# Performance work log

Measured on AMD Instinct MI355X. Metric: run time of the kernel, lower is better.

Reference implementation:

```python
import jax, jax.numpy as jnp
import numpy as np

B, C, G, P, W, H = 16, 64, 256, 4096, 1024, 256
WQ = W // 4  # wsi_dim // 4 = 256
D = C + G + WQ  # concat dim fed to score MLP = 576


def _init_linear(key, fan_in, fan_out):
    k1, k2 = jax.random.split(key)
    bound = 1.0 / np.sqrt(fan_in)
    w = jax.random.uniform(k1, (fan_in, fan_out), jnp.float32, -bound, bound)
    b = jax.random.uniform(k2, (fan_out,), jnp.float32, -bound, bound)
    return w, b


def setup_inputs() -> dict:
    key = jax.random.key(0)
    ks = jax.random.split(key, 8)
    cx = jax.random.normal(ks[0], (B, C), jnp.float32)
    gx = jax.random.normal(ks[1], (B, G), jnp.float32)
    wx = jax.random.normal(ks[2], (B, P, W), jnp.float32)
    Wc, bc = _init_linear(ks[3], C, C)        # fc_c
    Wg, bg = _init_linear(ks[4], G, G)        # fc_g
    Ww, bw = _init_linear(ks[5], W, WQ)       # fc_w
    W1, b1 = _init_linear(ks[6], D, H)        # FCLayers hidden
    W2, b2 = _init_linear(ks[7], H, 1)        # FCLayers out
    return {"cx": cx, "gx": gx, "wx": wx,
            "Wc": Wc, "bc": bc, "Wg": Wg, "bg": bg, "Ww": Ww, "bw": bw,
            "W1": W1, "b1": b1, "W2": W2, "b2": b2}


def reference(cx, gx, wx, Wc, bc, Wg, bg, Ww, bw, W1, b1, W2, b2):
    # Per-modality projections
    c = cx @ Wc + bc                      # [B, C]
    g = gx @ Wg + bg                      # [B, G]
    w = jnp.einsum('bpw,wq->bpq', wx, Ww) + bw  # [B, P, WQ]
    # Score MLP on concat(c, g, w_i) for every patch, vectorized by
    # splitting W1 rows over the concat blocks (avoids materializing concat):
    W1c, W1g, W1w = W1[:C], W1[C:C + G], W1[C + G:]
    h = jax.nn.relu((c @ W1c + g @ W1g + b1)[:, None, :]
                    + jnp.einsum('bpq,qh->bph', w, W1w))  # [B, P, H]
    scores = h @ W2 + b2                  # [B, P, 1]
    attn = jax.nn.softmax(scores, axis=1)  # softmax over patches
    return jnp.sum(attn * w, axis=1)      # [B, WQ]
```

## Files before the change

kernel.cpp:

```cpp
#include <hip/hip_runtime.h>
#include <hip/hip_bf16.h>

#define B_   16
#define C_   64
#define G_   256
#define P_   4096
#define W_   1024
#define H_   256
#define WQ_  256
#define M_   (B_ * P_)

typedef __attribute__((ext_vector_type(8))) _Float16 f16x8;
typedef __attribute__((ext_vector_type(4))) float    f32x4;

__device__ __forceinline__ float h2f(ushort u) {
    union { ushort u; _Float16 h; } cv; cv.u = u;
    return (float)cv.h;
}

#define GLOAD16(gsrc, ldst)                                                  \
    __builtin_amdgcn_global_load_lds(                                        \
        (const __attribute__((address_space(1))) unsigned int*)(gsrc),       \
        (__attribute__((address_space(3))) unsigned int*)(ldst), 16, 0, 0)

__device__ __forceinline__ void convT_dev(
    const float* __restrict__ src, ushort* __restrict__ dst,
    int K, int N, int blk, float* tile )
{
    const int nb = N >> 6;
    const int k0 = (blk / nb) * 64;
    const int n0 = (blk % nb) * 64;
    const int t = threadIdx.x;
    #pragma unroll
    for (int i = 0; i < 16; ++i) {
        int e = i * 256 + t;
        int kr = e >> 6, nc = e & 63;
        tile[nc * 65 + kr] = src[(size_t)(k0 + kr) * N + n0 + nc];
    }
    __syncthreads();
    #pragma unroll
    for (int i = 0; i < 16; ++i) {
        int e = i * 256 + t;
        int nc = e >> 6, kr = e & 63;
        union { _Float16 h; ushort u; } cv;
        cv.h = (_Float16)tile[nc * 65 + kr];
        dst[(size_t)(n0 + nc) * K + k0 + kr] = cv.u;
    }
}

__global__ __launch_bounds__(256) void setup_kernel(
    const float* __restrict__ Ww,  ushort* __restrict__ WwT,
    const float* __restrict__ W1w, ushort* __restrict__ W1T,
    const float* __restrict__ cx, const float* __restrict__ gx,
    const float* __restrict__ Wc, const float* __restrict__ bc,
    const float* __restrict__ Wg, const float* __restrict__ bg,
    const float* __restrict__ W1, const float* __restrict__ b1,
    float* __restrict__ base_out)
{
    __shared__ float smem[64 * 65];
    const int blk = blockIdx.x;
    if (blk < 64) {
        convT_dev(Ww, WwT, W_, WQ_, blk, smem);
        return;
    }
    if (blk < 80) {
        convT_dev(W1w, W1T, H_, H_, blk - 64, smem);
        return;
    }
    const int b = blk - 80;
    const int t = threadIdx.x;
    float* cxl = smem;
    float* gxl = smem + 64;
    float* cl  = smem + 320;
    float* gl  = smem + 384;

    if (t < C_) cxl[t] = cx[b * C_ + t];
    gxl[t] = gx[b * G_ + t];
    __syncthreads();

    if (t < C_) {
        float acc = bc[t];
        #pragma unroll 4
        for (int i = 0; i < C_; ++i) acc += cxl[i] * Wc[i * C_ + t];
        cl[t] = acc;
    }
    {
        float acc = bg[t];
        #pragma unroll 4
        for (int i = 0; i < G_; ++i) acc += gxl[i] * Wg[i * G_ + t];
        gl[t] = acc;
    }
    __syncthreads();

    float acc = b1[t];
    #pragma unroll 4
    for (int i = 0; i < C_; ++i) acc += cl[i] * W1[i * H_ + t];
    #pragma unroll 4
    for (int i = 0; i < G_; ++i) acc += gl[i] * W1[(C_ + i) * H_ + t];
    base_out[b * H_ + t] = acc;
}

__global__ __launch_bounds__(512, 2) void gemm_w_fused(
    const float* __restrict__ A,
    const ushort* __restrict__ BT,
    const float* __restrict__ bw,
    const ushort* __restrict__ W1T,
    const float* __restrict__ base_,
    const float* __restrict__ W2,
    const float* __restrict__ b2,
    ushort* Cout,
    float* __restrict__ scores)
{
    __shared__ __align__(16) char smem[65536];
    float*  Af = (float*)smem;
    ushort* Bh = (ushort*)(smem + 32768);
    ushort* wt = (ushort*)smem;

    const int t = threadIdx.x;
    const int row0 = blockIdx.x * 128;
    const int b = blockIdx.x >> 5;
    const int lane = t & 63, wave = t >> 6;
    const int wm = wave >> 2, wn = wave & 3;
    const int l15 = lane & 15, lq = lane >> 4;

    const float *srcA0, *srcA1, *srcA2, *srcA3;
    char *dstA0, *dstA1, *dstA2, *dstA3;
    {
        const int o0 = t * 16, o1 = o0 + 8192, o2 = o0 + 16384, o3 = o0 + 24576;
        const int r0 = o0 >> 8, r1 = o1 >> 8, r2 = o2 >> 8, r3 = o3 >> 8;
        srcA0 = A + (size_t)(row0 + r0) * W_ + (((o0 & 255) ^ ((r0 & 7) << 4)) >> 2);
        srcA1 = A + (size_t)(row0 + r1) * W_ + (((o1 & 255) ^ ((r1 & 7) << 4)) >> 2);
        srcA2 = A + (size_t)(row0 + r2) * W_ + (((o2 & 255) ^ ((r2 & 7) << 4)) >> 2);
        srcA3 = A + (size_t)(row0 + r3) * W_ + (((o3 & 255) ^ ((r3 & 7) << 4)) >> 2);
        dstA0 = (char*)Af + o0; dstA1 = (char*)Af + o1;
        dstA2 = (char*)Af + o2; dstA3 = (char*)Af + o3;
    }
    const ushort *srcB0, *srcB1, *srcB2, *srcB3;
    char *dstB0, *dstB1, *dstB2, *dstB3;
    {
        const int o0 = t * 16, o1 = o0 + 8192, o2 = o0 + 16384, o3 = o0 + 24576;
        const int c0 = o0 >> 7, c1 = o1 >> 7, c2 = o2 >> 7, c3 = o3 >> 7;
        srcB0 = BT + (size_t)c0 * W_ + (((o0 & 127) ^ ((c0 & 7) << 4)) >> 1);
        srcB1 = BT + (size_t)c1 * W_ + (((o1 & 127) ^ ((c1 & 7) << 4)) >> 1);
        srcB2 = BT + (size_t)c2 * W_ + (((o2 & 127) ^ ((c2 & 7) << 4)) >> 1);
        srcB3 = BT + (size_t)c3 * W_ + (((o3 & 127) ^ ((c3 & 7) << 4)) >> 1);
        dstB0 = (char*)Bh + o0; dstB1 = (char*)Bh + o1;
        dstB2 = (char*)Bh + o2; dstB3 = (char*)Bh + o3;
    }

    f32x4 acc[4][4];
    #pragma unroll
    for (int m = 0; m < 4; ++m)
        #pragma unroll
        for (int n = 0; n < 4; ++n) acc[m][n] = (f32x4){0.f, 0.f, 0.f, 0.f};

    for (int k0 = 0; k0 < W_; k0 += 64) {
        if (k0) __syncthreads();
        GLOAD16(srcA0 + k0, dstA0);
        GLOAD16(srcA1 + k0, dstA1);
        GLOAD16(srcA2 + k0, dstA2);
        GLOAD16(srcA3 + k0, dstA3);
        GLOAD16(srcB0 + k0, dstB0);
        GLOAD16(srcB1 + k0, dstB1);
        GLOAD16(srcB2 + k0, dstB2);
        GLOAD16(srcB3 + k0, dstB3);
        __syncthreads();

        #pragma unroll
        for (int ks = 0; ks < 2; ++ks) {
            f16x8 af[4], bf[4];
            #pragma unroll
            for (int m = 0; m < 4; ++m) {
                const int r = wm * 64 + m * 16 + l15;
                const int base = r * 256 + ks * 128 + lq * 32;
                const int swz  = (r & 7) << 4;
                const f32x4 a0 = *(const f32x4*)((const char*)Af + (base ^ swz));
                const f32x4 a1 = *(const f32x4*)((const char*)Af + ((base + 16) ^ swz));
                f16x8 h;
                h[0] = (_Float16)a0[0]; h[1] = (_Float16)a0[1];
                h[2] = (_Float16)a0[2]; h[3] = (_Float16)a0[3];
                h[4] = (_Float16)a1[0]; h[5] = (_Float16)a1[1];
                h[6] = (_Float16)a1[2]; h[7] = (_Float16)a1[3];
                af[m] = h;
            }
            #pragma unroll
            for (int n = 0; n < 4; ++n) {
                const int c = wn * 64 + n * 16 + l15;
                const int byte = (c * 128 + ks * 64 + lq * 16) ^ ((c & 7) << 4);
                bf[n] = *(const f16x8*)((const char*)Bh + byte);
            }
            #pragma unroll
            for (int m = 0; m < 4; ++m)
                #pragma unroll
                for (int n = 0; n < 4; ++n)
                    acc[m][n] = __builtin_amdgcn_mfma_f32_16x16x32_f16(
                        af[m], bf[n], acc[m][n], 0, 0, 0);
        }
    }

    __syncthreads();
    {
        float bwv[4];
        #pragma unroll
        for (int n = 0; n < 4; ++n) bwv[n] = bw[wn * 64 + n * 16 + l15];
        #pragma unroll
        for (int m = 0; m < 4; ++m)
            #pragma unroll
            for (int reg = 0; reg < 4; ++reg) {
                const int rl = wm * 64 + m * 16 + lq * 4 + reg;
                #pragma unroll
                for (int n = 0; n < 4; ++n) {
                    const int col = wn * 64 + n * 16 + l15;
                    union { _Float16 h; ushort u; } cv;
                    cv.h = (_Float16)(acc[m][n][reg] + bwv[n]);
                    Cout[(size_t)(row0 + rl) * WQ_ + col] = cv.u;
                    *(ushort*)((char*)wt + ((rl * 512 + col * 2) ^ ((rl & 7) << 4))) = cv.u;
                }
            }
    }
    __syncthreads();

    f32x4 acc2[4][4];
    #pragma unroll
    for (int m = 0; m < 4; ++m)
        #pragma unroll
        for (int n = 0; n < 4; ++n) acc2[m][n] = (f32x4){0.f, 0.f, 0.f, 0.f};

    for (int k2 = 0; k2 < WQ_; k2 += 32) {
        f16x8 af[4], bf[4];
        #pragma unroll
        for (int m = 0; m < 4; ++m) {
            const int r = wm * 64 + m * 16 + l15;
            const int byte = (r * 512 + (k2 + lq * 8) * 2) ^ ((r & 7) << 4);
            af[m] = *(const f16x8*)((const char*)wt + byte);
        }
        #pragma unroll
        for (int n = 0; n < 4; ++n) {
            const int c = wn * 64 + n * 16 + l15;
            bf[n] = *(const f16x8*)(W1T + (size_t)c * WQ_ + k2 + lq * 8);
        }
        #pragma unroll
        for (int m = 0; m < 4; ++m)
            #pragma unroll
            for (int n = 0; n < 4; ++n)
                acc2[m][n] = __builtin_amdgcn_mfma_f32_16x16x32_f16(
                    af[m], bf[n], acc2[m][n], 0, 0, 0);
    }

    __syncthreads();
    {
        float (*red2)[128] = (float(*)[128])smem;
        float basev[4], w2v[4];
        #pragma unroll
        for (int n = 0; n < 4; ++n) {
            const int col = wn * 64 + n * 16 + l15;
            basev[n] = base_[b * H_ + col];
            w2v[n] = W2[col];
        }
        #pragma unroll
        for (int m = 0; m < 4; ++m)
            #pragma unroll
            for (int reg = 0; reg < 4; ++reg) {
                float s = 0.f;
                #pragma unroll
                for (int n = 0; n < 4; ++n) {
                    float h = acc2[m][n][reg] + basev[n];
                    h = fmaxf(h, 0.f);
                    s += h * w2v[n];
                }
                s += __shfl_xor(s, 1, 64);
                s += __shfl_xor(s, 2, 64);
                s += __shfl_xor(s, 4, 64);
                s += __shfl_xor(s, 8, 64);
                if (l15 == 0) red2[wn][wm * 64 + m * 16 + lq * 4 + reg] = s;
            }
        __syncthreads();
        if (t < 128) {
            scores[row0 + t] =
                red2[0][t] + red2[1][t] + red2[2][t] + red2[3][t] + b2[0];
        }
    }
}

__global__ __launch_bounds__(256) void weighted_partial_kernel(
    const ushort* __restrict__ wmat16, const float* __restrict__ scores,
    float* __restrict__ part)
{
    const int blk = blockIdx.x;
    const int b   = blk >> 5;
    const int sl  = blk & 31;
    const int t   = threadIdx.x;
    const int rg  = t >> 5;
    const int q8  = (t & 31) * 8;
    __shared__ float red[8][WQ_];
    __shared__ float mred[4];

    float mv = -1e30f;
    for (int p = t; p < P_; p += 256) mv = fmaxf(mv, scores[b * P_ + p]);
    #pragma unroll
    for (int d = 1; d < 64; d <<= 1) mv = fmaxf(mv, __shfl_xor(mv, d, 64));
    if ((t & 63) == 0) mred[t >> 6] = mv;
    __syncthreads();
    const float m = fmaxf(fmaxf(mred[0], mred[1]), fmaxf(mred[2], mred[3]));

    float acc[8];
    #pragma unroll
    for (int j = 0; j < 8; ++j) acc[j] = 0.f;

    const int p0 = sl * 128 + rg * 16;
    for (int p = p0; p < p0 + 16; ++p) {
        const float e = expf(scores[b * P_ + p] - m);
        const uint4 raw = *(const uint4*)(wmat16 + ((size_t)b * P_ + p) * WQ_ + q8);
        const ushort* u = (const ushort*)&raw;
        #pragma unroll
        for (int j = 0; j < 8; ++j) acc[j] += e * h2f(u[j]);
    }
    #pragma unroll
    for (int j = 0; j < 8; ++j) red[rg][q8 + j] = acc[j];
    __syncthreads();
    float s = 0.f;
    #pragma unroll
    for (int g = 0; g < 8; ++g) s += red[g][t];
    part[(size_t)(b * 32 + sl) * WQ_ + t] = s;
}

__global__ __launch_bounds__(256) void finalize_kernel(
    const float* __restrict__ part, const float* __restrict__ scores,
    float* __restrict__ out)
{
    const int b = blockIdx.x;
    const int t = threadIdx.x;
    __shared__ float mred[4];
    __shared__ float zred[4];

    float mv = -1e30f;
    for (int p = t; p < P_; p += 256) mv = fmaxf(mv, scores[b * P_ + p]);
    #pragma unroll
    for (int d = 1; d < 64; d <<= 1) mv = fmaxf(mv, __shfl_xor(mv, d, 64));
    if ((t & 63) == 0) mred[t >> 6] = mv;
    __syncthreads();
    const float m = fmaxf(fmaxf(mred[0], mred[1]), fmaxf(mred[2], mred[3]));

    float zv = 0.f;
    for (int p = t; p < P_; p += 256) zv += expf(scores[b * P_ + p] - m);
    #pragma unroll
    for (int d = 1; d < 64; d <<= 1) zv += __shfl_xor(zv, d, 64);
    if ((t & 63) == 0) zred[t >> 6] = zv;
    __syncthreads();
    const float z = zred[0] + zred[1] + zred[2] + zred[3];

    float acc = 0.f;
    #pragma unroll
    for (int sl = 0; sl < 32; ++sl) acc += part[(size_t)(b * 32 + sl) * WQ_ + t];
    out[b * WQ_ + t] = acc / z;
}

extern "C" void kernel_launch(void* const* d_in, const int* in_sizes, int n_in,
                              void* d_out, int out_size, void* d_ws, size_t ws_size,
                              hipStream_t stream) {
    const float* cx = (const float*)d_in[0];
    const float* gx = (const float*)d_in[1];
    const float* wx = (const float*)d_in[2];
    const float* Wc = (const float*)d_in[3];
    const float* bc = (const float*)d_in[4];
    const float* Wg = (const float*)d_in[5];
    const float* bg = (const float*)d_in[6];
    const float* Ww = (const float*)d_in[7];
    const float* bw = (const float*)d_in[8];
    const float* W1 = (const float*)d_in[9];
    const float* b1 = (const float*)d_in[10];
    const float* W2 = (const float*)d_in[11];
    const float* b2 = (const float*)d_in[12];
    float* out = (float*)d_out;

    float* ws        = (float*)d_ws;
    ushort* ws_w16   = (ushort*)ws;
    float* ws_scores = ws + (size_t)M_ * WQ_ / 2;
    float* ws_base   = ws_scores + M_;
    float* ws_part   = ws_base + B_ * H_;
    ushort* WwT16    = (ushort*)(ws_part + B_ * 32 * WQ_);
    ushort* W1T16    = WwT16 + (size_t)W_ * WQ_;

    setup_kernel<<<96, 256, 0, stream>>>(
        Ww, WwT16, W1 + (size_t)(C_ + G_) * H_, W1T16,
        cx, gx, Wc, bc, Wg, bg, W1, b1, ws_base);

    gemm_w_fused<<<M_ / 128, 512, 0, stream>>>(
        wx, WwT16, bw, W1T16, ws_base, W2, b2, ws_w16, ws_scores);

    weighted_partial_kernel<<<B_ * 32, 256, 0, stream>>>(ws_w16, ws_scores, ws_part);

    finalize_kernel<<<B_, 256, 0, stream>>>(ws_part, ws_scores, out);
}
```

Measured before the change: 177.2 us.

## Double-buffer A/B tiles in fused GEMM with half-depth K stages

```diff
diff --git a/kernel.cpp b/kernel.cpp
--- a/kernel.cpp
+++ b/kernel.cpp
@@ -22,6 +22,13 @@
     __builtin_amdgcn_global_load_lds(                                        \
         (const __attribute__((address_space(1))) unsigned int*)(gsrc),       \
         (__attribute__((address_space(3))) unsigned int*)(ldst), 16, 0, 0)
+
+__device__ __forceinline__ int inv_swz64(int o) {
+    const int b8 = (o >> 8) & 1, b7 = (o >> 7) & 1, b6 = (o >> 6) & 1;
+    const int b5 = (o >> 5) & 1, b4 = (o >> 4) & 1;
+    const int l6 = b6 ^ b8, l5 = b5 ^ b7, l4 = b4 ^ l6;
+    return (o & ~0x70) | (l6 << 6) | (l5 << 5) | (l4 << 4);
+}
 
 __device__ __forceinline__ void convT_dev(
     const float* __restrict__ src, ushort* __restrict__ dst,
@@ -112,8 +119,6 @@
     float* __restrict__ scores)
 {
     __shared__ __align__(16) char smem[65536];
-    float*  Af = (float*)smem;
-    ushort* Bh = (ushort*)(smem + 32768);
     ushort* wt = (ushort*)smem;
 
     const int t = threadIdx.x;
@@ -123,29 +128,25 @@
     const int wm = wave >> 2, wn = wave & 3;
     const int l15 = lane & 15, lq = lane >> 4;
 
-    const float *srcA0, *srcA1, *srcA2, *srcA3;
-    char *dstA0, *dstA1, *dstA2, *dstA3;
-    {
-        const int o0 = t * 16, o1 = o0 + 8192, o2 = o0 + 16384, o3 = o0 + 24576;
-        const int r0 = o0 >> 8, r1 = o1 >> 8, r2 = o2 >> 8, r3 = o3 >> 8;
-        srcA0 = A + (size_t)(row0 + r0) * W_ + (((o0 & 255) ^ ((r0 & 7) << 4)) >> 2);
-        srcA1 = A + (size_t)(row0 + r1) * W_ + (((o1 & 255) ^ ((r1 & 7) << 4)) >> 2);
-        srcA2 = A + (size_t)(row0 + r2) * W_ + (((o2 & 255) ^ ((r2 & 7) << 4)) >> 2);
-        srcA3 = A + (size_t)(row0 + r3) * W_ + (((o3 & 255) ^ ((r3 & 7) << 4)) >> 2);
-        dstA0 = (char*)Af + o0; dstA1 = (char*)Af + o1;
-        dstA2 = (char*)Af + o2; dstA3 = (char*)Af + o3;
-    }
-    const ushort *srcB0, *srcB1, *srcB2, *srcB3;
-    char *dstB0, *dstB1, *dstB2, *dstB3;
-    {
-        const int o0 = t * 16, o1 = o0 + 8192, o2 = o0 + 16384, o3 = o0 + 24576;
-        const int c0 = o0 >> 7, c1 = o1 >> 7, c2 = o2 >> 7, c3 = o3 >> 7;
-        srcB0 = BT + (size_t)c0 * W_ + (((o0 & 127) ^ ((c0 & 7) << 4)) >> 1);
-        srcB1 = BT + (size_t)c1 * W_ + (((o1 & 127) ^ ((c1 & 7) << 4)) >> 1);
-        srcB2 = BT + (size_t)c2 * W_ + (((o2 & 127) ^ ((c2 & 7) << 4)) >> 1);
-        srcB3 = BT + (size_t)c3 * W_ + (((o3 & 127) ^ ((c3 & 7) << 4)) >> 1);
-        dstB0 = (char*)Bh + o0; dstB1 = (char*)Bh + o1;
-        dstB2 = (char*)Bh + o2; dstB3 = (char*)Bh + o3;
+    const int oA0 = t * 16, oA1 = t * 16 + 8192;
+    const int rA0 = oA0 >> 7, rA1 = oA1 >> 7;
+    const float* srcA0 = A + (size_t)(row0 + rA0) * W_
+                           + (((oA0 & 127) ^ ((rA0 & 7) << 4)) >> 2);
+    const float* srcA1 = A + (size_t)(row0 + rA1) * W_
+                           + (((oA1 & 127) ^ ((rA1 & 7) << 4)) >> 2);
+    const int oB0 = t * 16, oB1 = t * 16 + 8192;
+    const int lB0 = inv_swz64(oB0), lB1 = inv_swz64(oB1);
+    const ushort* srcB0 = BT + (size_t)(lB0 >> 6) * W_ + ((lB0 & 63) >> 1);
+    const ushort* srcB1 = BT + (size_t)(lB1 >> 6) * W_ + ((lB1 & 63) >> 1);
+
+#define STAGE1(BUF, K0)                                                      \
+    {                                                                        \
+        char* ab = smem + (BUF) * 16384;                                     \
+        char* bb = smem + 32768 + (BUF) * 16384;                             \
+        GLOAD16(srcA0 + (K0), ab + oA0);                                     \
+        GLOAD16(srcA1 + (K0), ab + oA1);                                     \
+        GLOAD16(srcB0 + (K0), bb + oB0);                                     \
+        GLOAD16(srcB1 + (K0), bb + oB1);                                     \
     }
 
     f32x4 acc[4][4];
@@ -154,51 +155,46 @@
         #pragma unroll
         for (int n = 0; n < 4; ++n) acc[m][n] = (f32x4){0.f, 0.f, 0.f, 0.f};
 
-    for (int k0 = 0; k0 < W_; k0 += 64) {
-        if (k0) __syncthreads();
-        GLOAD16(srcA0 + k0, dstA0);
-        GLOAD16(srcA1 + k0, dstA1);
-        GLOAD16(srcA2 + k0, dstA2);
-        GLOAD16(srcA3 + k0, dstA3);
-        GLOAD16(srcB0 + k0, dstB0);
-        GLOAD16(srcB1 + k0, dstB1);
-        GLOAD16(srcB2 + k0, dstB2);
-        GLOAD16(srcB3 + k0, dstB3);
+    STAGE1(0, 0)
+    __syncthreads();
+
+    for (int kt = 0; kt < 32; ++kt) {
+        const int cur = kt & 1;
+        if (kt + 1 < 32) STAGE1(cur ^ 1, (kt + 1) * 32)
+        const char* Af = smem + cur * 16384;
+        const char* Bh = smem + 32768 + cur * 16384;
+
+        f16x8 af[4], bf[4];
+        #pragma unroll
+        for (int m = 0; m < 4; ++m) {
+            const int r = wm * 64 + m * 16 + l15;
+            const int g = r * 128 + lq * 32;
+            const int swz = (r & 7) << 4;
+            const f32x4 a0 = *(const f32x4*)(Af + (g ^ swz));
+            const f32x4 a1 = *(const f32x4*)(Af + ((g + 16) ^ swz));
+            f16x8 h;
+            h[0] = (_Float16)a0[0]; h[1] = (_Float16)a0[1];
+            h[2] = (_Float16)a0[2]; h[3] = (_Float16)a0[3];
+            h[4] = (_Float16)a1[0]; h[5] = (_Float16)a1[1];
+            h[6] = (_Float16)a1[2]; h[7] = (_Float16)a1[3];
+            af[m] = h;
+        }
+        #pragma unroll
+        for (int n = 0; n < 4; ++n) {
+            const int c = wn * 64 + n * 16 + l15;
+            const int byte = (c * 64 + lq * 16) ^ ((c & 7) << 4);
+            bf[n] = *(const f16x8*)(Bh + byte);
+        }
+        #pragma unroll
+        for (int m = 0; m < 4; ++m)
+            #pragma unroll
+            for (int n = 0; n < 4; ++n)
+                acc[m][n] = __builtin_amdgcn_mfma_f32_16x16x32_f16(
+                    af[m], bf[n], acc[m][n], 0, 0, 0);
         __syncthreads();
-
-        #pragma unroll
-        for (int ks = 0; ks < 2; ++ks) {
-            f16x8 af[4], bf[4];
-            #pragma unroll
-            for (int m = 0; m < 4; ++m) {
-                const int r = wm * 64 + m * 16 + l15;
-                const int base = r * 256 + ks * 128 + lq * 32;
-                const int swz  = (r & 7) << 4;
-                const f32x4 a0 = *(const f32x4*)((const char*)Af + (base ^ swz));
-                const f32x4 a1 = *(const f32x4*)((const char*)Af + ((base + 16) ^ swz));
-                f16x8 h;
-                h[0] = (_Float16)a0[0]; h[1] = (_Float16)a0[1];
-                h[2] = (_Float16)a0[2]; h[3] = (_Float16)a0[3];
-                h[4] = (_Float16)a1[0]; h[5] = (_Float16)a1[1];
-                h[6] = (_Float16)a1[2]; h[7] = (_Float16)a1[3];
-                af[m] = h;
-            }
-            #pragma unroll
-            for (int n = 0; n < 4; ++n) {
-                const int c = wn * 64 + n * 16 + l15;
-                const int byte = (c * 128 + ks * 64 + lq * 16) ^ ((c & 7) << 4);
-                bf[n] = *(const f16x8*)((const char*)Bh + byte);
-            }
-            #pragma unroll
-            for (int m = 0; m < 4; ++m)
-                #pragma unroll
-                for (int n = 0; n < 4; ++n)
-                    acc[m][n] = __builtin_amdgcn_mfma_f32_16x16x32_f16(
-                        af[m], bf[n], acc[m][n], 0, 0, 0);
-        }
-    }
-
-    __syncthreads();
+    }
+#undef STAGE1
+
     {
         float bwv[4];
         #pragma unroll
```

New measurement: 183.5 us. 3.6% more time.

## Split fused projection+score GEMM into two kernels with LDS-staged score GEMM

Applied to the files above, without the earlier changes.

```diff
diff --git a/kernel.cpp b/kernel.cpp
--- a/kernel.cpp
+++ b/kernel.cpp
@@ -23,6 +23,13 @@
         (const __attribute__((address_space(1))) unsigned int*)(gsrc),       \
         (__attribute__((address_space(3))) unsigned int*)(ldst), 16, 0, 0)
 
+__device__ __forceinline__ int inv_swz64(int o) {
+    const int b8 = (o >> 8) & 1, b7 = (o >> 7) & 1, b6 = (o >> 6) & 1;
+    const int b5 = (o >> 5) & 1, b4 = (o >> 4) & 1;
+    const int l6 = b6 ^ b8, l5 = b5 ^ b7, l4 = b4 ^ l6;
+    return (o & ~0x70) | (l6 << 6) | (l5 << 5) | (l4 << 4);
+}
+
 __device__ __forceinline__ void convT_dev(
     const float* __restrict__ src, ushort* __restrict__ dst,
     int K, int N, int blk, float* tile )
@@ -100,25 +107,18 @@
     base_out[b * H_ + t] = acc;
 }
 
-__global__ __launch_bounds__(512, 2) void gemm_w_fused(
+__global__ __launch_bounds__(512, 2) void gemm_w_mfma(
     const float* __restrict__ A,
     const ushort* __restrict__ BT,
     const float* __restrict__ bw,
-    const ushort* __restrict__ W1T,
-    const float* __restrict__ base_,
-    const float* __restrict__ W2,
-    const float* __restrict__ b2,
-    ushort* Cout,
-    float* __restrict__ scores)
+    ushort* __restrict__ Cout)
 {
     __shared__ __align__(16) char smem[65536];
     float*  Af = (float*)smem;
     ushort* Bh = (ushort*)(smem + 32768);
-    ushort* wt = (ushort*)smem;
 
     const int t = threadIdx.x;
     const int row0 = blockIdx.x * 128;
-    const int b = blockIdx.x >> 5;
     const int lane = t & 63, wave = t >> 6;
     const int wm = wave >> 2, wn = wave & 3;
     const int l15 = lane & 15, lq = lane >> 4;
@@ -198,87 +198,115 @@
         }
     }
 
-    __syncthreads();
-    {
-        float bwv[4];
-        #pragma unroll
-        for (int n = 0; n < 4; ++n) bwv[n] = bw[wn * 64 + n * 16 + l15];
-        #pragma unroll
-        for (int m = 0; m < 4; ++m)
-            #pragma unroll
-            for (int reg = 0; reg < 4; ++reg) {
-                const int rl = wm * 64 + m * 16 + lq * 4 + reg;
-                #pragma unroll
-                for (int n = 0; n < 4; ++n) {
-                    const int col = wn * 64 + n * 16 + l15;
-                    union { _Float16 h; ushort u; } cv;
-                    cv.h = (_Float16)(acc[m][n][reg] + bwv[n]);
-                    Cout[(size_t)(row0 + rl) * WQ_ + col] = cv.u;
-                    *(ushort*)((char*)wt + ((rl * 512 + col * 2) ^ ((rl & 7) << 4))) = cv.u;
-                }
+    float bwv[4];
+    #pragma unroll
+    for (int n = 0; n < 4; ++n) bwv[n] = bw[wn * 64 + n * 16 + l15];
+    #pragma unroll
+    for (int m = 0; m < 4; ++m)
+        #pragma unroll
+        for (int reg = 0; reg < 4; ++reg) {
+            const size_t r = (size_t)row0 + wm * 64 + m * 16 + lq * 4 + reg;
+            #pragma unroll
+            for (int n = 0; n < 4; ++n) {
+                union { _Float16 h; ushort u; } cv;
+                cv.h = (_Float16)(acc[m][n][reg] + bwv[n]);
+                Cout[r * WQ_ + wn * 64 + n * 16 + l15] = cv.u;
             }
-    }
-    __syncthreads();
-
-    f32x4 acc2[4][4];
+        }
+}
+
+__global__ __launch_bounds__(512) void gemm_scores_mfma(
+    const ushort* __restrict__ A16,
+    const ushort* __restrict__ BT,
+    const float* __restrict__ base_,
+    const float* __restrict__ W2,
+    const float* __restrict__ b2,
+    float* __restrict__ scores)
+{
+    __shared__ __align__(16) ushort Ah[128 * 32];
+    __shared__ __align__(16) ushort Bh[256 * 32];
+    __shared__ float red[4][128];
+    const int t = threadIdx.x;
+    const int row0 = blockIdx.x * 128;
+    const int b = blockIdx.x >> 5;
+    const int lane = t & 63, wave = t >> 6;
+    const int wm = wave >> 2, wn = wave & 3;
+    const int l15 = lane & 15, lq = lane >> 4;
+
+    const int oA = t * 16;
+    const int lA = inv_swz64(oA);
+    const ushort* srcA = A16 + (size_t)(row0 + (lA >> 6)) * H_ + ((lA & 63) >> 1);
+    char* dstA = (char*)Ah + oA;
+
+    const int oB0 = t * 16, oB1 = t * 16 + 8192;
+    const int lB0 = inv_swz64(oB0), lB1 = inv_swz64(oB1);
+    const ushort* srcB0 = BT + (size_t)(lB0 >> 6) * H_ + ((lB0 & 63) >> 1);
+    const ushort* srcB1 = BT + (size_t)(lB1 >> 6) * H_ + ((lB1 & 63) >> 1);
+    char* dstB0 = (char*)Bh + oB0;
+    char* dstB1 = (char*)Bh + oB1;
+
+    f32x4 acc[4][4];
     #pragma unroll
     for (int m = 0; m < 4; ++m)
         #pragma unroll
-        for (int n = 0; n < 4; ++n) acc2[m][n] = (f32x4){0.f, 0.f, 0.f, 0.f};
-
-    for (int k2 = 0; k2 < WQ_; k2 += 32) {
+        for (int n = 0; n < 4; ++n) acc[m][n] = (f32x4){0.f, 0.f, 0.f, 0.f};
+
+    for (int k0 = 0; k0 < H_; k0 += 32) {
+        if (k0) __syncthreads();
+        GLOAD16(srcA + k0, dstA);
+        GLOAD16(srcB0 + k0, dstB0);
+        GLOAD16(srcB1 + k0, dstB1);
+        __syncthreads();
+
         f16x8 af[4], bf[4];
         #pragma unroll
         for (int m = 0; m < 4; ++m) {
             const int r = wm * 64 + m * 16 + l15;
-            const int byte = (r * 512 + (k2 + lq * 8) * 2) ^ ((r & 7) << 4);
-            af[m] = *(const f16x8*)((const char*)wt + byte);
+            const int byte = (r * 64 + lq * 16) ^ ((r & 7) << 4);
+            af[m] = *(const f16x8*)((const char*)Ah + byte);
         }
         #pragma unroll
         for (int n = 0; n < 4; ++n) {
             const int c = wn * 64 + n * 16 + l15;
-            bf[n] = *(const f16x8*)(W1T + (size_t)c * WQ_ + k2 + lq * 8);
+            const int byte = (c * 64 + lq * 16) ^ ((c & 7) << 4);
+            bf[n] = *(const f16x8*)((const char*)Bh + byte);
         }
         #pragma unroll
         for (int m = 0; m < 4; ++m)
             #pragma unroll
             for (int n = 0; n < 4; ++n)
-                acc2[m][n] = __builtin_amdgcn_mfma_f32_16x16x32_f16(
-                    af[m], bf[n], acc2[m][n], 0, 0, 0);
-    }
-
-    __syncthreads();
-    {
-        float (*red2)[128] = (float(*)[128])smem;
-        float basev[4], w2v[4];
-        #pragma unroll
-        for (int n = 0; n < 4; ++n) {
-            const int col = wn * 64 + n * 16 + l15;
-            basev[n] = base_[b * H_ + col];
-            w2v[n] = W2[col];
+                acc[m][n] = __builtin_amdgcn_mfma_f32_16x16x32_f16(
+                    af[m], bf[n], acc[m][n], 0, 0, 0);
+    }
+
+    float basev[4], w2v[4];
+    #pragma unroll
+    for (int n = 0; n < 4; ++n) {
+        const int col = wn * 64 + n * 16 + l15;
+        basev[n] = base_[b * H_ + col];
+        w2v[n] = W2[col];
+    }
+    __syncthreads();
+    #pragma unroll
+    for (int m = 0; m < 4; ++m)
+        #pragma unroll
+        for (int reg = 0; reg < 4; ++reg) {
+            float s = 0.f;
+            #pragma unroll
+            for (int n = 0; n < 4; ++n) {
+                float h = acc[m][n][reg] + basev[n];
+                h = fmaxf(h, 0.f);
+                s += h * w2v[n];
+            }
+            s += __shfl_xor(s, 1, 64);
+            s += __shfl_xor(s, 2, 64);
+            s += __shfl_xor(s, 4, 64);
+            s += __shfl_xor(s, 8, 64);
+            if (l15 == 0) red[wn][wm * 64 + m * 16 + lq * 4 + reg] = s;
         }
-        #pragma unroll
-        for (int m = 0; m < 4; ++m)
-            #pragma unroll
-            for (int reg = 0; reg < 4; ++reg) {
-                float s = 0.f;
-                #pragma unroll
-                for (int n = 0; n < 4; ++n) {
-                    float h = acc2[m][n][reg] + basev[n];
-                    h = fmaxf(h, 0.f);
-                    s += h * w2v[n];
-                }
-                s += __shfl_xor(s, 1, 64);
-                s += __shfl_xor(s, 2, 64);
-                s += __shfl_xor(s, 4, 64);
-                s += __shfl_xor(s, 8, 64);
-                if (l15 == 0) red2[wn][wm * 64 + m * 16 + lq * 4 + reg] = s;
-            }
-        __syncthreads();
-        if (t < 128) {
-            scores[row0 + t] =
-                red2[0][t] + red2[1][t] + red2[2][t] + red2[3][t] + b2[0];
-        }
+    __syncthreads();
+    if (t < 128) {
+        scores[row0 + t] = red[0][t] + red[1][t] + red[2][t] + red[3][t] + b2[0];
     }
 }
 
@@ -385,8 +413,10 @@
         Ww, WwT16, W1 + (size_t)(C_ + G_) * H_, W1T16,
         cx, gx, Wc, bc, Wg, bg, W1, b1, ws_base);
 
-    gemm_w_fused<<<M_ / 128, 512, 0, stream>>>(
-        wx, WwT16, bw, W1T16, ws_base, W2, b2, ws_w16, ws_scores);
+    gemm_w_mfma<<<M_ / 128, 512, 0, stream>>>(wx, WwT16, bw, ws_w16);
+
+    gemm_scores_mfma<<<M_ / 128, 512, 0, stream>>>(
+        ws_w16, W1T16, ws_base, W2, b2, ws_scores);
 
     weighted_partial_kernel<<<B_ * 32, 256, 0, stream>>>(ws_w16, ws_scores, ws_part);
 
```

Result: no change. 176.8 us (-0.2%).
